# Performance work log

Hardware: AMD Instinct MI355X
Metric: run time of the kernel (lower is better)

## Reference

```python
import jax, jax.numpy as jnp
import numpy as np

N_NODES = 50000
N_EDGES = 800000
X_DIM = 128         # node feature dim
HID = 128           # hidden_channels == edge_attr channels
IN_CH = X_DIM + HID # MLP in_channels = 256
OUT_CH = 128


def setup_inputs() -> dict:
    key = jax.random.key(0)
    ks = jax.random.split(key, 10)
    x = jax.random.normal(ks[0], (N_NODES, X_DIM), dtype=jnp.float32)
    edge_index = jax.random.randint(ks[1], (2, N_EDGES), 0, N_NODES, dtype=jnp.int64)
    edge_attr = jax.random.normal(ks[2], (N_EDGES, HID), dtype=jnp.float32)
    # MLP params (stored as [in, out]); scale like torch Linear default init
    def lin(k, fan_in, fan_out):
        k1, k2 = jax.random.split(k)
        bound = 1.0 / np.sqrt(fan_in)
        W = jax.random.uniform(k1, (fan_in, fan_out), minval=-bound, maxval=bound, dtype=jnp.float32)
        b = jax.random.uniform(k2, (fan_out,), minval=-bound, maxval=bound, dtype=jnp.float32)
        return W, b
    W0, b0 = lin(ks[3], IN_CH, HID)
    W2, b2 = lin(ks[4], HID, HID)
    W3, b3 = lin(ks[5], HID, OUT_CH)
    return {"x": x, "edge_index": edge_index, "edge_attr": edge_attr,
            "W0": W0, "b0": b0, "W2": W2, "b2": b2, "W3": W3, "b3": b3}


def reference(x, edge_index, edge_attr, W0, b0, W2, b2, W3, b3):
    # edge_sum[n, c] = sum over edges e with edge_index[0, e] == n of edge_attr[e, c]
    # (equivalent to the per-channel sparse COO @ ones loop, fused across channels)
    edge_sum = jax.ops.segment_sum(edge_attr, edge_index[0], num_segments=x.shape[0])
    inputs = jnp.concatenate([x, edge_sum], axis=1)  # [N, in_channels]
    h = jax.nn.elu(inputs @ W0 + b0)
    h = jax.nn.elu(h @ W2 + b2)
    out = h @ W3 + b3
    return out
```

## Files before the change

kernel.cpp:

```cpp
#include <hip/hip_runtime.h>
#include <cmath>

typedef __attribute__((ext_vector_type(8))) short bf16x8;
typedef __attribute__((ext_vector_type(4))) float f32x4;

__device__ __forceinline__ short f2bf(float f) {
    unsigned u = __builtin_bit_cast(unsigned, f);
    u += 0x7fff + ((u >> 16) & 1);
    return (short)(u >> 16);
}

__global__ __launch_bounds__(256)
void hist_kernel(const int* __restrict__ dst, int* __restrict__ counts, int E)
{
    int e = blockIdx.x * 256 + threadIdx.x;
    if (e < E) atomicAdd(&counts[dst[e]], 1);
}

#define SCAN_B 256

__global__ __launch_bounds__(SCAN_B)
void scan_p1_kernel(const int* __restrict__ counts, int* __restrict__ offsets,
                    int* __restrict__ blockSums, int N)
{
    __shared__ int sh[SCAN_B];
    const int t = threadIdx.x;
    const int i = blockIdx.x * SCAN_B + t;
    int v = (i < N) ? counts[i] : 0;
    sh[t] = v;
    __syncthreads();
    for (int d = 1; d < SCAN_B; d <<= 1) {
        int u = (t >= d) ? sh[t - d] : 0;
        __syncthreads();
        sh[t] += u;
        __syncthreads();
    }
    if (i < N) offsets[i] = sh[t] - v;
    if (t == SCAN_B - 1) blockSums[blockIdx.x] = sh[SCAN_B - 1];
}

__global__ __launch_bounds__(SCAN_B)
void scan_p2_kernel(int* __restrict__ blockSums, int nblk)
{
    __shared__ int sh[SCAN_B];
    const int t = threadIdx.x;
    int v = (t < nblk) ? blockSums[t] : 0;
    sh[t] = v;
    __syncthreads();
    for (int d = 1; d < SCAN_B; d <<= 1) {
        int u = (t >= d) ? sh[t - d] : 0;
        __syncthreads();
        sh[t] += u;
        __syncthreads();
    }
    if (t < nblk) blockSums[t] = sh[t] - v;
}

__global__ __launch_bounds__(SCAN_B)
void scan_p3_kernel(int* __restrict__ offsets, const int* __restrict__ blockSums,
                    int* __restrict__ cursor, int N, int E)
{
    const int i = blockIdx.x * SCAN_B + threadIdx.x;
    if (i < N) {
        int o = offsets[i] + blockSums[blockIdx.x];
        offsets[i] = o;
        cursor[i]  = o;
    }
    if (i == 0) offsets[N] = E;
}

__global__ __launch_bounds__(256)
void scatter_perm_kernel(const int* __restrict__ dst, int* __restrict__ cursor,
                         int* __restrict__ perm, int E)
{
    int e = blockIdx.x * 256 + threadIdx.x;
    if (e < E) {
        int p = atomicAdd(&cursor[dst[e]], 1);
        perm[p] = e;
    }
}

__global__ __launch_bounds__(256)
void gather_bf16_kernel(const float* __restrict__ edge_attr,
                        const int* __restrict__ perm,
                        const int* __restrict__ offsets,
                        unsigned short* __restrict__ esB, int N, int total)
{
    const int wid  = (blockIdx.x * 256 + threadIdx.x) >> 6;
    const int lane = threadIdx.x & 63;
    if (wid >= total) return;
    const int half = lane >> 5;
    const int li   = lane & 31;

    float4 acc = make_float4(0.f, 0.f, 0.f, 0.f);
    if (wid < N) {
        const int beg = offsets[wid];
        const int end = offsets[wid + 1];
        for (int base = beg; base < end; base += 64) {
            const int m = (end - base < 64) ? (end - base) : 64;
            int eid = 0;
            if (lane < m) eid = perm[base + lane];
            const int pairs = (m + 1) >> 1;
            #pragma unroll 4
            for (int j = 0; j < pairs; ++j) {
                const int idx = 2 * j + half;
                const int e = __shfl(eid, idx, 64);
                if (idx < m) {
                    const float4 v = *reinterpret_cast<const float4*>(
                        &edge_attr[(size_t)e * 128 + li * 4]);
                    acc.x += v.x; acc.y += v.y; acc.z += v.z; acc.w += v.w;
                }
            }
        }
    }
    float4 o;
    o.x = __shfl(acc.x, li + 32, 64);
    o.y = __shfl(acc.y, li + 32, 64);
    o.z = __shfl(acc.z, li + 32, 64);
    o.w = __shfl(acc.w, li + 32, 64);
    if (half == 0) {
        acc.x += o.x; acc.y += o.y; acc.z += o.z; acc.w += o.w;
        const int r   = wid & 127;
        const int t   = wid >> 7;
        const int grp = (li >> 1) ^ (r & 15);
        ushort4 s;
        s.x = (unsigned short)f2bf(acc.x);
        s.y = (unsigned short)f2bf(acc.y);
        s.z = (unsigned short)f2bf(acc.z);
        s.w = (unsigned short)f2bf(acc.w);
        *reinterpret_cast<ushort4*>(
            &esB[(size_t)t * 16384 + r * 128 + grp * 8 + (li & 1) * 4]) = s;
    }
}

__device__ __forceinline__ void stage_W(const float* __restrict__ W, int krow0,
                                        short* __restrict__ Wt, int tid)
{
    #pragma unroll
    for (int i = 0; i < 16; ++i) {
        int p = tid + i * 512;
        int n = p & 127;
        int k = (p >> 7) << 1;
        float a = W[(size_t)(krow0 + k) * 128 + n];
        float b = W[(size_t)(krow0 + k + 1) * 128 + n];
        int grp = (k >> 3) ^ (n & 15);
        ushort2 s;
        s.x = (unsigned short)f2bf(a);
        s.y = (unsigned short)f2bf(b);
        *reinterpret_cast<ushort2*>(&Wt[n * 128 + grp * 8 + (k & 7)]) = s;
    }
}

__global__ __launch_bounds__(512, 2)
void fused_mlp_kernel(const float* __restrict__ x,
                      const unsigned short* __restrict__ esB,
                      const float* __restrict__ W0, const float* __restrict__ b0,
                      const float* __restrict__ W2, const float* __restrict__ b2,
                      const float* __restrict__ W3, const float* __restrict__ b3,
                      float* __restrict__ out, int N)
{
    __shared__ short At[128 * 128];
    __shared__ short Wt[128 * 128];

    const int tid  = threadIdx.x;
    const int lane = tid & 63;
    const int wv   = tid >> 6;
    const int l15  = lane & 15;
    const int quad = lane >> 4;
    const int m0   = wv * 16;
    const int blockRow = blockIdx.x * 128;

    f32x4 acc[8];
    #pragma unroll
    for (int nt = 0; nt < 8; ++nt) acc[nt] = (f32x4){0.f, 0.f, 0.f, 0.f};

    uint4 es[4];
    {
        const uint4* esg = reinterpret_cast<const uint4*>(esB) +
                           (size_t)blockIdx.x * 2048;
        #pragma unroll
        for (int i = 0; i < 4; ++i) es[i] = esg[i * 512 + tid];
    }

    #pragma unroll
    for (int i = 0; i < 8; ++i) {
        int f  = tid + i * 512;
        int r  = f >> 5;
        int c4 = (f & 31) << 2;
        int g  = blockRow + r; if (g >= N) g = N - 1;
        const float4 v = *reinterpret_cast<const float4*>(&x[(size_t)g * 128 + c4]);
        int grp = (c4 >> 3) ^ (r & 15);
        ushort4 s;
        s.x = (unsigned short)f2bf(v.x);
        s.y = (unsigned short)f2bf(v.y);
        s.z = (unsigned short)f2bf(v.z);
        s.w = (unsigned short)f2bf(v.w);
        *reinterpret_cast<ushort4*>(&At[r * 128 + grp * 8 + (c4 & 7)]) = s;
    }
    stage_W(W0, 0, Wt, tid);
    __syncthreads();
    #pragma unroll
    for (int ks = 0; ks < 4; ++ks) {
        int g = ks * 4 + quad;
        int so = ((g ^ l15) << 3);
        bf16x8 a = *reinterpret_cast<bf16x8*>(&At[(m0 + l15) * 128 + so]);
        #pragma unroll
        for (int nt = 0; nt < 8; ++nt) {
            bf16x8 b = *reinterpret_cast<bf16x8*>(&Wt[(nt * 16 + l15) * 128 + so]);
            acc[nt] = __builtin_amdgcn_mfma_f32_16x16x32_bf16(a, b, acc[nt], 0, 0, 0);
        }
    }
    __syncthreads();

    {
        uint4* atv = reinterpret_cast<uint4*>(At);
        #pragma unroll
        for (int i = 0; i < 4; ++i) atv[i * 512 + tid] = es[i];
    }
    stage_W(W0, 128, Wt, tid);
    __syncthreads();
    #pragma unroll
    for (int ks = 0; ks < 4; ++ks) {
        int g = ks * 4 + quad;
        int so = ((g ^ l15) << 3);
        bf16x8 a = *reinterpret_cast<bf16x8*>(&At[(m0 + l15) * 128 + so]);
        #pragma unroll
        for (int nt = 0; nt < 8; ++nt) {
            bf16x8 b = *reinterpret_cast<bf16x8*>(&Wt[(nt * 16 + l15) * 128 + so]);
            acc[nt] = __builtin_amdgcn_mfma_f32_16x16x32_bf16(a, b, acc[nt], 0, 0, 0);
        }
    }

    __syncthreads();
    #pragma unroll
    for (int nt = 0; nt < 8; ++nt) {
        float bv = b0[nt * 16 + l15];
        #pragma unroll
        for (int r = 0; r < 4; ++r) {
            float v = acc[nt][r] + bv;
            v = (v > 0.f) ? v : (__expf(v) - 1.f);
            int m = m0 + quad * 4 + r;
            int c = nt * 16 + l15;
            int grp = (c >> 3) ^ (m & 15);
            At[m * 128 + grp * 8 + (c & 7)] = f2bf(v);
        }
        acc[nt] = (f32x4){0.f, 0.f, 0.f, 0.f};
    }
    stage_W(W2, 0, Wt, tid);
    __syncthreads();

    #pragma unroll
    for (int ks = 0; ks < 4; ++ks) {
        int g = ks * 4 + quad;
        int so = ((g ^ l15) << 3);
        bf16x8 a = *reinterpret_cast<bf16x8*>(&At[(m0 + l15) * 128 + so]);
        #pragma unroll
        for (int nt = 0; nt < 8; ++nt) {
            bf16x8 b = *reinterpret_cast<bf16x8*>(&Wt[(nt * 16 + l15) * 128 + so]);
            acc[nt] = __builtin_amdgcn_mfma_f32_16x16x32_bf16(a, b, acc[nt], 0, 0, 0);
        }
    }

    __syncthreads();
    #pragma unroll
    for (int nt = 0; nt < 8; ++nt) {
        float bv = b2[nt * 16 + l15];
        #pragma unroll
        for (int r = 0; r < 4; ++r) {
            float v = acc[nt][r] + bv;
            v = (v > 0.f) ? v : (__expf(v) - 1.f);
            int m = m0 + quad * 4 + r;
            int c = nt * 16 + l15;
            int grp = (c >> 3) ^ (m & 15);
            At[m * 128 + grp * 8 + (c & 7)] = f2bf(v);
        }
        acc[nt] = (f32x4){0.f, 0.f, 0.f, 0.f};
    }
    stage_W(W3, 0, Wt, tid);
    __syncthreads();

    #pragma unroll
    for (int ks = 0; ks < 4; ++ks) {
        int g = ks * 4 + quad;
        int so = ((g ^ l15) << 3);
        bf16x8 a = *reinterpret_cast<bf16x8*>(&At[(m0 + l15) * 128 + so]);
        #pragma unroll
        for (int nt = 0; nt < 8; ++nt) {
            bf16x8 b = *reinterpret_cast<bf16x8*>(&Wt[(nt * 16 + l15) * 128 + so]);
            acc[nt] = __builtin_amdgcn_mfma_f32_16x16x32_bf16(a, b, acc[nt], 0, 0, 0);
        }
    }

    #pragma unroll
    for (int nt = 0; nt < 8; ++nt) {
        float bv = b3[nt * 16 + l15];
        #pragma unroll
        for (int r = 0; r < 4; ++r) {
            int gr = blockRow + m0 + quad * 4 + r;
            if (gr < N) out[(size_t)gr * 128 + nt * 16 + l15] = acc[nt][r] + bv;
        }
    }
}

extern "C" void kernel_launch(void* const* d_in, const int* in_sizes, int n_in,
                              void* d_out, int out_size, void* d_ws, size_t ws_size,
                              hipStream_t stream)
{
    const float* x     = (const float*)d_in[0];
    const int*   eidx  = (const int*)d_in[1];
    const float* eattr = (const float*)d_in[2];
    const float* W0 = (const float*)d_in[3];
    const float* b0 = (const float*)d_in[4];
    const float* W2 = (const float*)d_in[5];
    const float* b2 = (const float*)d_in[6];
    const float* W3 = (const float*)d_in[7];
    const float* b3 = (const float*)d_in[8];
    float* out = (float*)d_out;

    const int N = in_sizes[0] / 128;
    const int E = in_sizes[2] / 128;

    int* counts    = (int*)d_ws;
    int* offsets   = counts + N;
    int* cursor    = offsets + (N + 1);
    int* blockSums = cursor + N;
    int* perm      = blockSums + 256;
    uintptr_t p = (uintptr_t)(perm + E);
    p = (p + 255) & ~(uintptr_t)255;
    unsigned short* esB = (unsigned short*)p;

    hipMemsetAsync(counts, 0, (size_t)N * sizeof(int), stream);

    const int eblocks = (E + 255) / 256;
    const int nblk    = (N + SCAN_B - 1) / SCAN_B;
    const int mblocks = (N + 127) / 128;
    const int total   = mblocks * 128;

    hist_kernel<<<eblocks, 256, 0, stream>>>(eidx, counts, E);
    scan_p1_kernel<<<nblk, SCAN_B, 0, stream>>>(counts, offsets, blockSums, N);
    scan_p2_kernel<<<1, SCAN_B, 0, stream>>>(blockSums, nblk);
    scan_p3_kernel<<<nblk, SCAN_B, 0, stream>>>(offsets, blockSums, cursor, N, E);
    scatter_perm_kernel<<<eblocks, 256, 0, stream>>>(eidx, cursor, perm, E);
    {
        int gthreads = total * 64;
        int gblocks  = (gthreads + 255) / 256;
        gather_bf16_kernel<<<gblocks, 256, 0, stream>>>(eattr, perm, offsets,
                                                        esB, N, total);
    }
    fused_mlp_kernel<<<mblocks, 512, 0, stream>>>(x, esB, W0, b0, W2, b2,
                                                  W3, b3, out, N);
}
```

Baseline: 699.6 us.

## Pre-convert weights to swizzled bf16 once and prefetch per-layer tiles in MLP

Adds a small kernel that converts W0, W2 and W3 to bf16 once per call, in the swizzled LDS layout, and stores them in workspace. The fused MLP now copies these tiles with vector loads, prefetching the next layer's weights into registers while the current layer computes. Before, each of the ~391 blocks re-read the fp32 weights with strided loads and converted them. Nontemporal loads and stores are also applied to edge_attr, x, esB and the output. The cost is one extra kernel launch and more register pressure from holding the prefetched weights.

```diff
diff --git a/kernel.cpp b/kernel.cpp
--- a/kernel.cpp
+++ b/kernel.cpp
@@ -3,11 +3,17 @@
 
 typedef __attribute__((ext_vector_type(8))) short bf16x8;
 typedef __attribute__((ext_vector_type(4))) float f32x4;
+typedef __attribute__((ext_vector_type(4))) unsigned int u32x4;
 
 __device__ __forceinline__ short f2bf(float f) {
     unsigned u = __builtin_bit_cast(unsigned, f);
     u += 0x7fff + ((u >> 16) & 1);
     return (short)(u >> 16);
+}
+
+__device__ __forceinline__ float4 ntload4(const float* p) {
+    f32x4 v = __builtin_nontemporal_load(reinterpret_cast<const f32x4*>(p));
+    return make_float4(v.x, v.y, v.z, v.w);
 }
 
 __global__ __launch_bounds__(256)
@@ -77,6 +83,34 @@
     if (e < E) {
         int p = atomicAdd(&cursor[dst[e]], 1);
         perm[p] = e;
+    }
+}
+
+__global__ __launch_bounds__(512)
+void convert_w_kernel(const float* __restrict__ W0, const float* __restrict__ W2,
+                      const float* __restrict__ W3, unsigned short* __restrict__ wB)
+{
+    const int tile = blockIdx.x >> 3;
+    const int seg  = blockIdx.x & 7;
+    const float* W; int krow0;
+    if (tile == 0)      { W = W0; krow0 = 0; }
+    else if (tile == 1) { W = W0; krow0 = 128; }
+    else if (tile == 2) { W = W2; krow0 = 0; }
+    else                { W = W3; krow0 = 0; }
+    unsigned short* dst = wB + (size_t)tile * 16384;
+    const int tid = threadIdx.x;
+    #pragma unroll
+    for (int ii = 0; ii < 2; ++ii) {
+        int p = tid + (seg * 2 + ii) * 512;
+        int n = p & 127;
+        int k = (p >> 7) << 1;
+        float a = W[(size_t)(krow0 + k) * 128 + n];
+        float b = W[(size_t)(krow0 + k + 1) * 128 + n];
+        int grp = (k >> 3) ^ (n & 15);
+        ushort2 s;
+        s.x = (unsigned short)f2bf(a);
+        s.y = (unsigned short)f2bf(b);
+        *reinterpret_cast<ushort2*>(&dst[n * 128 + grp * 8 + (k & 7)]) = s;
     }
 }
 
@@ -106,8 +140,7 @@
                 const int idx = 2 * j + half;
                 const int e = __shfl(eid, idx, 64);
                 if (idx < m) {
-                    const float4 v = *reinterpret_cast<const float4*>(
-                        &edge_attr[(size_t)e * 128 + li * 4]);
+                    const float4 v = ntload4(&edge_attr[(size_t)e * 128 + li * 4]);
                     acc.x += v.x; acc.y += v.y; acc.z += v.z; acc.w += v.w;
                 }
             }
@@ -133,30 +166,26 @@
     }
 }
 
-__device__ __forceinline__ void stage_W(const float* __restrict__ W, int krow0,
-                                        short* __restrict__ Wt, int tid)
-{
-    #pragma unroll
-    for (int i = 0; i < 16; ++i) {
-        int p = tid + i * 512;
-        int n = p & 127;
-        int k = (p >> 7) << 1;
-        float a = W[(size_t)(krow0 + k) * 128 + n];
-        float b = W[(size_t)(krow0 + k + 1) * 128 + n];
-        int grp = (k >> 3) ^ (n & 15);
-        ushort2 s;
-        s.x = (unsigned short)f2bf(a);
-        s.y = (unsigned short)f2bf(b);
-        *reinterpret_cast<ushort2*>(&Wt[n * 128 + grp * 8 + (k & 7)]) = s;
-    }
+__device__ __forceinline__ void ldW(const u32x4* __restrict__ wt, u32x4* wreg, int tid)
+{
+    #pragma unroll
+    for (int i = 0; i < 4; ++i) wreg[i] = wt[i * 512 + tid];
+}
+
+__device__ __forceinline__ void stW(short* __restrict__ Wt, const u32x4* wreg, int tid)
+{
+    u32x4* wv = reinterpret_cast<u32x4*>(Wt);
+    #pragma unroll
+    for (int i = 0; i < 4; ++i) wv[i * 512 + tid] = wreg[i];
 }
 
 __global__ __launch_bounds__(512, 2)
 void fused_mlp_kernel(const float* __restrict__ x,
                       const unsigned short* __restrict__ esB,
-                      const float* __restrict__ W0, const float* __restrict__ b0,
-                      const float* __restrict__ W2, const float* __restrict__ b2,
-                      const float* __restrict__ W3, const float* __restrict__ b3,
+                      const unsigned short* __restrict__ wB,
+                      const float* __restrict__ b0,
+                      const float* __restrict__ b2,
+                      const float* __restrict__ b3,
                       float* __restrict__ out, int N)
 {
     __shared__ short At[128 * 128];
@@ -174,13 +203,18 @@
     #pragma unroll
     for (int nt = 0; nt < 8; ++nt) acc[nt] = (f32x4){0.f, 0.f, 0.f, 0.f};
 
-    uint4 es[4];
+    const u32x4* wb4 = reinterpret_cast<const u32x4*>(wB);
+
+    u32x4 es[4];
     {
-        const uint4* esg = reinterpret_cast<const uint4*>(esB) +
+        const u32x4* esg = reinterpret_cast<const u32x4*>(esB) +
                            (size_t)blockIdx.x * 2048;
         #pragma unroll
-        for (int i = 0; i < 4; ++i) es[i] = esg[i * 512 + tid];
-    }
+        for (int i = 0; i < 4; ++i)
+            es[i] = __builtin_nontemporal_load(&esg[i * 512 + tid]);
+    }
+    u32x4 wreg[4];
+    ldW(wb4 + 0 * 2048, wreg, tid);
 
     #pragma unroll
     for (int i = 0; i < 8; ++i) {
@@ -188,7 +222,7 @@
         int r  = f >> 5;
         int c4 = (f & 31) << 2;
         int g  = blockRow + r; if (g >= N) g = N - 1;
-        const float4 v = *reinterpret_cast<const float4*>(&x[(size_t)g * 128 + c4]);
+        const float4 v = ntload4(&x[(size_t)g * 128 + c4]);
         int grp = (c4 >> 3) ^ (r & 15);
         ushort4 s;
         s.x = (unsigned short)f2bf(v.x);
@@ -197,8 +231,9 @@
         s.w = (unsigned short)f2bf(v.w);
         *reinterpret_cast<ushort4*>(&At[r * 128 + grp * 8 + (c4 & 7)]) = s;
     }
-    stage_W(W0, 0, Wt, tid);
-    __syncthreads();
+    stW(Wt, wreg, tid);
+    __syncthreads();
+    ldW(wb4 + 1 * 2048, wreg, tid);
     #pragma unroll
     for (int ks = 0; ks < 4; ++ks) {
         int g = ks * 4 + quad;
@@ -213,12 +248,13 @@
     __syncthreads();
 
     {
-        uint4* atv = reinterpret_cast<uint4*>(At);
+        u32x4* atv = reinterpret_cast<u32x4*>(At);
         #pragma unroll
         for (int i = 0; i < 4; ++i) atv[i * 512 + tid] = es[i];
     }
-    stage_W(W0, 128, Wt, tid);
-    __syncthreads();
+    stW(Wt, wreg, tid);
+    __syncthreads();
+    ldW(wb4 + 2 * 2048, wreg, tid);
     #pragma unroll
     for (int ks = 0; ks < 4; ++ks) {
         int g = ks * 4 + quad;
@@ -246,8 +282,9 @@
         }
         acc[nt] = (f32x4){0.f, 0.f, 0.f, 0.f};
     }
-    stage_W(W2, 0, Wt, tid);
-    __syncthreads();
+    stW(Wt, wreg, tid);
+    __syncthreads();
+    ldW(wb4 + 3 * 2048, wreg, tid);
 
     #pragma unroll
     for (int ks = 0; ks < 4; ++ks) {
@@ -276,7 +313,7 @@
         }
         acc[nt] = (f32x4){0.f, 0.f, 0.f, 0.f};
     }
-    stage_W(W3, 0, Wt, tid);
+    stW(Wt, wreg, tid);
     __syncthreads();
 
     #pragma unroll
@@ -297,7 +334,9 @@
         #pragma unroll
         for (int r = 0; r < 4; ++r) {
             int gr = blockRow + m0 + quad * 4 + r;
-            if (gr < N) out[(size_t)gr * 128 + nt * 16 + l15] = acc[nt][r] + bv;
+            if (gr < N)
+                __builtin_nontemporal_store(acc[nt][r] + bv,
+                                            &out[(size_t)gr * 128 + nt * 16 + l15]);
         }
     }
 }
@@ -328,14 +367,18 @@
     uintptr_t p = (uintptr_t)(perm + E);
     p = (p + 255) & ~(uintptr_t)255;
     unsigned short* esB = (unsigned short*)p;
+    const int mblocks = (N + 127) / 128;
+    p = (uintptr_t)(esB + (size_t)mblocks * 16384);
+    p = (p + 255) & ~(uintptr_t)255;
+    unsigned short* wB = (unsigned short*)p;
 
     hipMemsetAsync(counts, 0, (size_t)N * sizeof(int), stream);
 
     const int eblocks = (E + 255) / 256;
     const int nblk    = (N + SCAN_B - 1) / SCAN_B;
-    const int mblocks = (N + 127) / 128;
     const int total   = mblocks * 128;
 
+    convert_w_kernel<<<32, 512, 0, stream>>>(W0, W2, W3, wB);
     hist_kernel<<<eblocks, 256, 0, stream>>>(eidx, counts, E);
     scan_p1_kernel<<<nblk, SCAN_B, 0, stream>>>(counts, offsets, blockSums, N);
     scan_p2_kernel<<<1, SCAN_B, 0, stream>>>(blockSums, nblk);
@@ -347,6 +390,5 @@
         gather_bf16_kernel<<<gblocks, 256, 0, stream>>>(eattr, perm, offsets,
                                                         esB, N, total);
     }
-    fused_mlp_kernel<<<mblocks, 512, 0, stream>>>(x, esB, W0, b0, W2, b2,
-                                                  W3, b3, out, N);
-}
+    fused_mlp_kernel<<<mblocks, 512, 0, stream>>>(x, esB, wB, b0, b2, b3, out, N);
+}
```

After: 665.9 us. -4.8%, faster.
